# Kernel optimization log

Hardware: AMD Instinct MI355X
Metric: run time of the kernel (lower is better)

## Reference

```python
import jax, jax.numpy as jnp
import numpy as np

H_IMG = 256; W_IMG = 256; C = 256
WIN = (16, 16); STRIPE = (32, 32); DF = 4; NH = 4
ASZ = (STRIPE[0] // DF, STRIPE[1] // DF)
TS = ((STRIPE[0] + ASZ[0]) // 2, (STRIPE[1] + ASZ[1]) // 2)  # stripe bias table half-size (20,20)


def _win_part(x, ws):
    # (B,H,W,c) -> (B*nW, ws0*ws1, c)
    B, H, W, c = x.shape
    x = x.reshape(B, H // ws[0], ws[0], W // ws[1], ws[1], c)
    return x.transpose(0, 1, 3, 2, 4, 5).reshape(-1, ws[0] * ws[1], c)


def _win_rev(w, ws, H, W):
    c = w.shape[-1]
    B = w.shape[0] // ((H // ws[0]) * (W // ws[1]))
    x = w.reshape(B, H // ws[0], W // ws[1], ws[0], ws[1], c)
    return x.transpose(0, 1, 3, 2, 4, 5).reshape(B, H, W, c)


def _l2n(x):
    # F.normalize(dim=-1)
    return x / jnp.maximum(jnp.linalg.norm(x, axis=-1, keepdims=True), 1e-12)


def _affine(attn, logit_scale, w1, b1, w2, table, index):
    # attn: (B_, nH, N1, N2); AffineTransform with mask=None
    N1, N2 = attn.shape[-2], attn.shape[-1]
    attn = attn * jnp.exp(jnp.minimum(logit_scale, np.log(100.0)))  # clamp max=log(1/0.01)
    bt = jax.nn.relu(table.reshape(-1, 2) @ w1 + b1) @ w2  # (T, nH)
    bias = bt[index.reshape(-1)].reshape(N1, N2, -1).transpose(2, 0, 1)  # (nH,N1,N2)
    return attn + (16.0 * jax.nn.sigmoid(bias))[None]


def _coords(start, size):
    h = np.arange(start[0], start[0] + size[0])
    w = np.arange(start[1], start[1] + size[1])
    return np.stack(np.meshgrid(h, w, indexing='ij')).reshape(2, -1)


def _idx(c1, c2, md):
    d = (c1[:, :, None] - c2[:, None, :]).transpose(1, 2, 0).astype(np.int64)
    return (d[..., 0] + md[0] - 1) * (2 * md[1] - 1) + (d[..., 1] + md[1] - 1)


def _table(ts):
    h = np.arange(-(ts[0] - 1), ts[0], dtype=np.float32) / (ts[0] - 1)
    w = np.arange(-(ts[1] - 1), ts[1], dtype=np.float32) / (ts[1] - 1)
    t = np.stack(np.meshgrid(h, w, indexing='ij'), axis=-1)[None] * 8.0
    return (np.sign(t) * np.log2(np.abs(t) + 1.0) / np.log2(8.0)).astype(np.float32)


def setup_inputs():
    ks = iter(jax.random.split(jax.random.key(0), 32))
    def nrm(shape, s=0.02):
        return jax.random.normal(next(ks), shape, dtype=jnp.float32) * s
    inp = {}
    inp['x'] = jax.random.normal(next(ks), (1, H_IMG * W_IMG, C), dtype=jnp.float32)
    inp['qkv_w'] = nrm((C, 3 * C)); inp['qkv_b'] = nrm((3 * C,))
    inp['anchor_w'] = nrm((C, C // 2)); inp['anchor_b'] = nrm((C // 2,))
    for tag in ['w', 's1', 's2']:
        inp['ls_' + tag] = jnp.full((NH, 1, 1), np.log(10.0), dtype=jnp.float32)
        inp['cpb_w1_' + tag] = nrm((2, 512), 0.1)
        inp['cpb_b1_' + tag] = nrm((512,), 0.1)
        inp['cpb_w2_' + tag] = nrm((512, NH), 0.1)
    inp['proj_w'] = nrm((C, C)); inp['proj_b'] = nrm((C,))
    inp['table_w'] = jnp.asarray(_table(WIN))
    inp['table_s'] = jnp.asarray(_table(TS))
    cw = _coords((0, 0), WIN)
    inp['index_w'] = jnp.asarray(_idx(cw, cw, WIN), dtype=jnp.int32)
    cs = _coords((0, 0), STRIPE)
    st = ((STRIPE[0] - ASZ[0]) // 2, (STRIPE[1] - ASZ[1]) // 2)
    ca = _coords(st, ASZ)
    inp['index_a2w'] = jnp.asarray(_idx(ca, cs, TS), dtype=jnp.int32)
    inp['index_w2a'] = jnp.asarray(_idx(cs, ca, TS), dtype=jnp.int32)
    return inp


def reference(x, qkv_w, qkv_b, anchor_w, anchor_b,
              ls_w, cpb_w1_w, cpb_b1_w, cpb_w2_w,
              ls_s1, cpb_w1_s1, cpb_b1_s1, cpb_w2_s1,
              ls_s2, cpb_w1_s2, cpb_b1_s2, cpb_w2_s2,
              proj_w, proj_b, table_w, table_s,
              index_w, index_a2w, index_w2a):
    B, L, c = x.shape
    qkv = x @ qkv_w + qkv_b               # (B, L, 3C)
    half = 3 * c // 2
    hd = half // 3 // NH                  # head_dim per branch
    # ---- window attention on first half of qkv channels ----
    qw = _win_part(qkv[..., :half].reshape(B, H_IMG, W_IMG, half), WIN)  # (B_, N, 3*C/2)
    B_, N, _ = qw.shape
    q, k, v = qw.reshape(B_, N, 3, NH, hd).transpose(2, 0, 3, 1, 4)
    attn = jnp.einsum('bhnd,bhmd->bhnm', _l2n(q), _l2n(k))
    attn = jax.nn.softmax(_affine(attn, ls_w, cpb_w1_w, cpb_b1_w, cpb_w2_w, table_w, index_w), axis=-1)
    xw = jnp.einsum('bhnm,bhmd->bhnd', attn, v).transpose(0, 2, 1, 3).reshape(B_, N, NH * hd)
    xw = _win_rev(xw, WIN, H_IMG, W_IMG).reshape(B, L, c // 2)
    # ---- anchor projection: AvgPool2d(DF) + Linear(C -> C/2) ----
    xi = x.reshape(B, H_IMG, W_IMG, c)
    pooled = xi.reshape(B, H_IMG // DF, DF, W_IMG // DF, DF, c).mean(axis=(2, 4))
    anchor = pooled @ anchor_w + anchor_b  # (B, H/DF, W/DF, C/2)
    # ---- anchor stripe attention on second half ----
    qs = _win_part(qkv[..., half:].reshape(B, H_IMG, W_IMG, half), STRIPE)  # (Bs, N1, 3*C/2)
    Bs, N1, _ = qs.shape
    anc = _win_part(anchor, ASZ)           # (Bs, N2, C/2)
    N2 = anc.shape[1]
    q, k, v = qs.reshape(Bs, N1, 3, NH, hd).transpose(2, 0, 3, 1, 4)
    anc = anc.reshape(Bs, N2, NH, hd).transpose(0, 2, 1, 3)
    a1 = jnp.einsum('bhnd,bhmd->bhnm', _l2n(anc), _l2n(k))   # (Bs,NH,N2,N1)
    a1 = jax.nn.softmax(_affine(a1, ls_s1, cpb_w1_s1, cpb_b1_s1, cpb_w2_s1, table_s, index_a2w), axis=-1)
    xm = jnp.einsum('bhnm,bhmd->bhnd', a1, v)                # (Bs,NH,N2,hd)
    a2 = jnp.einsum('bhnd,bhmd->bhnm', _l2n(q), _l2n(anc))   # (Bs,NH,N1,N2)
    a2 = jax.nn.softmax(_affine(a2, ls_s2, cpb_w1_s2, cpb_b1_s2, cpb_w2_s2, table_s, index_w2a), axis=-1)
    xs = jnp.einsum('bhnm,bhmd->bhnd', a2, xm).transpose(0, 2, 1, 3).reshape(Bs, N1, NH * hd)
    xs = _win_rev(xs, STRIPE, H_IMG, W_IMG).reshape(B, L, c // 2)
    # ---- merge + output projection ----
    return jnp.concatenate([xw, xs], axis=-1) @ proj_w + proj_b
```

## Files before the change

### kernel.cpp

```cpp
#include <hip/hip_runtime.h>
#include <cstdint>
#include <cstddef>

typedef unsigned short u16;
typedef __attribute__((ext_vector_type(8))) short short8;
typedef __attribute__((ext_vector_type(4))) float floatx4;
typedef __attribute__((ext_vector_type(2))) float floatx2;
typedef __attribute__((ext_vector_type(4))) unsigned int uintx4;
typedef __attribute__((ext_vector_type(2))) unsigned int uintx2;
typedef __attribute__((ext_vector_type(2))) __bf16 bf16x2;

#define LOG2E 1.44269504f

__device__ __forceinline__ float bf2f(u16 u){
  union { unsigned int i; float f; } v; v.i = ((unsigned int)u) << 16; return v.f;
}
__device__ __forceinline__ u16 f2bf(float f){
  union { __bf16 b; u16 u; } v; v.b = (__bf16)f; return v.u;
}
__device__ __forceinline__ unsigned int pk2(float a, float b){
  union { bf16x2 h; unsigned int u; } v;
  v.h = __builtin_convertvector((floatx2){a, b}, bf16x2);
  return v.u;
}
__device__ __forceinline__ void gload16(const void* g, void* l){
  __builtin_amdgcn_global_load_lds((const __attribute__((address_space(1))) unsigned int*)g,
                                   (__attribute__((address_space(3))) unsigned int*)l, 16, 0, 0);
}
__device__ __forceinline__ float redq(float v){
  v += __shfl_xor(v, 16); v += __shfl_xor(v, 32);
  return v;
}

__global__ void transpose_w(const float* __restrict__ qkv_w, const float* __restrict__ anchor_w,
                            const float* __restrict__ proj_w,
                            u16* __restrict__ qkvt, u16* __restrict__ anct, u16* __restrict__ projt){
  int id = blockIdx.x*256 + threadIdx.x;
  if (id < 196608){ int k = id / 768, n = id % 768; qkvt[n*256 + k] = f2bf(qkv_w[id]); }
  else if (id < 229376){ int r = id - 196608; int k = r / 128, n = r % 128; anct[n*256 + k] = f2bf(anchor_w[r]); }
  else { int r = id - 229376; int k = r >> 8, n = r & 255; projt[n*256 + k] = f2bf(proj_w[r]); }
}

__global__ void cpb_mlp(const float* __restrict__ tw, const float* __restrict__ ts,
                        const float* __restrict__ w1w, const float* __restrict__ b1w, const float* __restrict__ w2w,
                        const float* __restrict__ w1s1, const float* __restrict__ b1s1, const float* __restrict__ w2s1,
                        const float* __restrict__ w1s2, const float* __restrict__ b1s2, const float* __restrict__ w2s2,
                        float* __restrict__ btw, float* __restrict__ bts1, float* __restrict__ bts2){
  int tag = blockIdx.y;
  const float *tab, *w1, *b1, *w2; float* bt; int T;
  if (tag == 0){ tab = tw; w1 = w1w;  b1 = b1w;  w2 = w2w;  bt = btw;  T = 961; }
  else if (tag == 1){ tab = ts; w1 = w1s1; b1 = b1s1; w2 = w2s1; bt = bts1; T = 1521; }
  else { tab = ts; w1 = w1s2; b1 = b1s2; w2 = w2s2; bt = bts2; T = 1521; }
  __shared__ float sw1[2][512];
  __shared__ float sb1[512];
  __shared__ float sw2[512][4];
  for (int j = threadIdx.x; j < 512; j += 256){
    sw1[0][j] = w1[j]; sw1[1][j] = w1[512 + j]; sb1[j] = b1[j];
    for (int h = 0; h < 4; ++h) sw2[j][h] = w2[j*4 + h];
  }
  __syncthreads();
  int idx = blockIdx.x*256 + threadIdx.x;
  int r = idx >> 2, hh = idx & 3;
  if (r < T){
    float t0 = tab[2*r], t1 = tab[2*r + 1];
    float acc = 0.f;
    for (int j = 0; j < 512; ++j){
      float hj = fmaxf(fmaf(t0, sw1[0][j], fmaf(t1, sw1[1][j], sb1[j])), 0.f);
      acc = fmaf(hj, sw2[j][hh], acc);
    }
    bt[r*4 + hh] = acc;
  }
}

__global__ void bias_gather(const float* __restrict__ btw, const float* __restrict__ bts1,
                            const float* __restrict__ bts2,
                            const int* __restrict__ idxw, const int* __restrict__ idxa2w,
                            const int* __restrict__ idxw2a,
                            const float* __restrict__ lsw, const float* __restrict__ ls1,
                            const float* __restrict__ ls2,
                            float* __restrict__ bw, float* __restrict__ bs1, float* __restrict__ bs2){
  int id = blockIdx.x*256 + threadIdx.x;
  int which = id >> 18;
  int rem = id & 262143;
  int h = rem >> 16, e = rem & 65535;
  const float* bt; const int* ix; float* dst; const float* ls;
  if (which == 0){ bt = btw;  ix = idxw;   dst = bw;  ls = lsw; }
  else if (which == 1){ bt = bts1; ix = idxa2w; dst = bs1; ls = ls1; }
  else { bt = bts2; ix = idxw2a; dst = bs2; ls = ls2; }
  float v = bt[ix[e]*4 + h];
  float scale = exp2f(fminf(ls[h], 4.6051702f) * LOG2E);
  float off = fminf(scale + 16.f, 80.f);
  float sig = 16.f / (1.f + exp2f(-v * LOG2E));
  float out = (sig - off) * LOG2E;
  int idx;
  if (which == 0){
    int q = e >> 8, k = e & 255;
    idx = ((((h*8 + (k>>5))*2 + ((k>>4)&1))*4 + ((k>>2)&3)) << 10) + (q << 2) + (k & 3);
  } else if (which == 1){
    int a = e >> 10, k = e & 1023;
    idx = (((h*64 + (k>>4))*4 + ((k>>2)&3)) << 8) + (a << 2) + (k & 3);
  } else {
    int q = e >> 6, k = e & 63;
    idx = (((h*4 + (k>>4))*4 + ((k>>2)&3)) << 12) + (q << 2) + (k & 3);
  }
  dst[idx] = out;
}

__global__ void avgpool(const float* __restrict__ x, u16* __restrict__ xb,
                        u16* __restrict__ pooledb){
  int a = blockIdx.x, c = threadIdx.x;
  int ay = a >> 6, ax = a & 63;
  float acc = 0.f;
#pragma unroll
  for (int dy = 0; dy < 4; ++dy)
#pragma unroll
    for (int dx = 0; dx < 4; ++dx){
      int row = (ay*4 + dy)*256 + ax*4 + dx;
      float v = x[(size_t)row*256 + c];
      xb[(size_t)row*256 + c] = f2bf(v);
      acc += v;
    }
  pooledb[(size_t)a*256 + c] = f2bf(acc * 0.0625f);
}

__launch_bounds__(256, 2)
__global__ void gemm_bf(const u16* __restrict__ A, const u16* __restrict__ Bt,
                        const float* __restrict__ bias, u16* __restrict__ CW,
                        u16* __restrict__ CS, int Nstr, int nyb, int normSl){
  __shared__ __align__(16) u16 lsA[2][4096];
  __shared__ __align__(16) u16 lsB[2][4096];
  const int tid = threadIdx.x, lane = tid & 63, wv = tid >> 6;
  const int lane15 = lane & 15, quad = lane >> 4;
  const int wr = wv >> 1, wc = wv & 1;
  const int m0 = blockIdx.x * 128;
  const int y = blockIdx.y;
  const int br = y / nyb, sl = y - br*nyb;
  u16* C = br ? CS : CW;
  const int srow = wv*16 + (lane >> 2), sk = (lane & 3)*8;
  const u16* as = A + (size_t)(m0 + srow)*256 + sk;
  const u16* bs = Bt + (size_t)(y*128 + srow)*256 + sk;
  auto stage = [&](int kw, int buf){
    char* dA = (char*)lsA[buf]; char* dB = (char*)lsB[buf];
    gload16(as + kw*32,            dA + wv*1024);
    gload16(as + 64*256 + kw*32,   dA + 4096 + wv*1024);
    gload16(bs + kw*32,            dB + wv*1024);
    gload16(bs + 64*256 + kw*32,   dB + 4096 + wv*1024);
  };
  stage(0, 0);
  floatx4 acc[4][4] = {};
  for (int kw = 0; kw < 8; ++kw){
    __syncthreads();
    if (kw < 7) stage(kw + 1, (kw + 1) & 1);
    const char* Ac = (const char*)lsA[kw & 1];
    const char* Bc = (const char*)lsB[kw & 1];
    short8 a[4], b[4];
#pragma unroll
    for (int i = 0; i < 4; ++i)
      a[i] = *(const short8*)(Ac + (wr*64 + i*16 + lane15)*64 + quad*16);
#pragma unroll
    for (int j = 0; j < 4; ++j)
      b[j] = *(const short8*)(Bc + (wc*64 + j*16 + lane15)*64 + quad*16);
#pragma unroll
    for (int i = 0; i < 4; ++i)
#pragma unroll
      for (int j = 0; j < 4; ++j)
        acc[i][j] = __builtin_amdgcn_mfma_f32_16x16x32_bf16(b[j], a[i], acc[i][j], 0, 0, 0);
  }
#pragma unroll
  for (int j = 0; j < 4; ++j){
    floatx4 bz = *(const floatx4*)(bias + y*128 + wc*64 + j*16 + quad*4);
#pragma unroll
    for (int i = 0; i < 4; ++i) acc[i][j] += bz;
  }
  if (sl < normSl){
#pragma unroll
    for (int i = 0; i < 4; ++i)
#pragma unroll
      for (int jp = 0; jp < 2; ++jp){
        floatx4 s2 = acc[i][jp*2]*acc[i][jp*2] + acc[i][jp*2+1]*acc[i][jp*2+1];
        float ss = (s2.x + s2.y) + (s2.z + s2.w);
        ss = redq(ss);
        float inv = 1.f / fmaxf(sqrtf(ss), 1e-12f);
        acc[i][jp*2]   *= inv;
        acc[i][jp*2+1] *= inv;
      }
  }
#pragma unroll
  for (int i = 0; i < 4; ++i){
    int row = m0 + wr*64 + i*16 + lane15;
#pragma unroll
    for (int j = 0; j < 4; ++j){
      int colb = sl*128 + wc*64 + j*16 + quad*4;
      uintx2 w;
      w.x = pk2(acc[i][j][0], acc[i][j][1]);
      w.y = pk2(acc[i][j][2], acc[i][j][3]);
      *(uintx2*)(C + (size_t)row*Nstr + colb) = w;
    }
  }
}

__launch_bounds__(256, 2)
__global__ void gemm_proj(const u16* __restrict__ Ab, const u16* __restrict__ Bt,
                          const float* __restrict__ bias, float* __restrict__ Cout){
  __shared__ __align__(16) u16 lsA[2][4096];
  __shared__ __align__(16) u16 lsB[2][8192];
  const int tid = threadIdx.x, lane = tid & 63, wv = tid >> 6;
  const int lane15 = lane & 15, quad = lane >> 4;
  const int wr = wv >> 1, wc = wv & 1;
  const int m0 = blockIdx.x * 128;
  const int srow = wv*16 + (lane >> 2), sk = (lane & 3)*8;
  const u16* as = Ab + (size_t)(m0 + srow)*256 + sk;
  const u16* bs = Bt + (size_t)srow*256 + sk;
  auto stage = [&](int kw, int buf){
    char* dA = (char*)lsA[buf]; char* dB = (char*)lsB[buf];
    gload16(as + kw*32,             dA + wv*1024);
    gload16(as + 64*256 + kw*32,    dA + 4096  + wv*1024);
    gload16(bs + kw*32,             dB + wv*1024);
    gload16(bs + 64*256 + kw*32,    dB + 4096  + wv*1024);
    gload16(bs + 128*256 + kw*32,   dB + 8192  + wv*1024);
    gload16(bs + 192*256 + kw*32,   dB + 12288 + wv*1024);
  };
  stage(0, 0);
  floatx4 acc[4][8] = {};
  for (int kw = 0; kw < 8; ++kw){
    __syncthreads();
    if (kw < 7) stage(kw + 1, (kw + 1) & 1);
    const char* Ac = (const char*)lsA[kw & 1];
    const char* Bc = (const char*)lsB[kw & 1];
    short8 a[4], b[8];
#pragma unroll
    for (int i = 0; i < 4; ++i)
      a[i] = *(const short8*)(Ac + (wr*64 + i*16 + lane15)*64 + quad*16);
#pragma unroll
    for (int j = 0; j < 8; ++j)
      b[j] = *(const short8*)(Bc + (wc*128 + j*16 + lane15)*64 + quad*16);
#pragma unroll
    for (int i = 0; i < 4; ++i)
#pragma unroll
      for (int j = 0; j < 8; ++j)
        acc[i][j] = __builtin_amdgcn_mfma_f32_16x16x32_bf16(b[j], a[i], acc[i][j], 0, 0, 0);
  }
#pragma unroll
  for (int i = 0; i < 4; ++i){
    int row = m0 + wr*64 + i*16 + lane15;
#pragma unroll
    for (int j = 0; j < 8; ++j){
      int colb = wc*128 + j*16 + quad*4;
      floatx4 bz = *(const floatx4*)(bias + colb);
      floatx4 o = acc[i][j] + bz;
      *(floatx4*)(Cout + (size_t)row*256 + colb) = o;
    }
  }
}

__launch_bounds__(256, 3)
__global__ void win_attn(const u16* __restrict__ qkvh, const float* __restrict__ lsw,
                         const float* __restrict__ biasw, u16* __restrict__ outm){
  __shared__ __align__(16) u16 sm[24832];
  const int tid = threadIdx.x, lane = tid & 63, wv = tid >> 6;
  const int lane15 = lane & 15, quad = lane >> 4;
  const int h = blockIdx.y;
  const int wyl = blockIdx.x >> 4, wx = blockIdx.x & 15;
  u16* Ks = sm;
  u16* Qs = sm + 8192;
  u16* VT = sm + 16384;
  {
    int tok = wv*64 + lane;
    int row = (wyl*16 + (tok >> 4))*256 + wx*16 + (tok & 15);
    const char* src = (const char*)qkvh + (size_t)row*768 + h*64;
#pragma unroll
    for (int kq = 0; kq < 4; ++kq){
      gload16(src + kq*16,        (char*)Qs + wv*1024 + kq*4096);
      gload16(src + 256 + kq*16,  (char*)Ks + wv*1024 + kq*4096);
    }
    int vrow = (wyl*16 + (tid >> 4))*256 + wx*16 + (tid & 15);
    const uintx4* vp = (const uintx4*)((const char*)qkvh + (size_t)vrow*768 + 512 + h*64);
    uintx4 v0 = vp[0], v1 = vp[1], v2 = vp[2], v3 = vp[3];
    unsigned int w[16] = {v0.x,v0.y,v0.z,v0.w, v1.x,v1.y,v1.z,v1.w,
                          v2.x,v2.y,v2.z,v2.w, v3.x,v3.y,v3.z,v3.w};
    u16* vd = VT + (tid >> 3)*264 + (tid & 7);
#pragma unroll
    for (int c = 0; c < 16; ++c){
      vd[(c*2)*8]   = (u16)(w[c] & 0xffffu);
      vd[(c*2+1)*8] = (u16)(w[c] >> 16);
    }
  }
  __syncthreads();
  short8 qf[4];
#pragma unroll
  for (int j = 0; j < 4; ++j)
    qf[j] = *(const short8*)(Qs + quad*2048 + (wv*64 + j*16 + lane15)*8);
  __syncthreads();

  float scale = exp2f(fminf(lsw[h], 4.6051702f) * LOG2E) * LOG2E;
  u16* Pw = Qs + wv*2048;
  const floatx4 zf4 = {0.f, 0.f, 0.f, 0.f};
  floatx4 accO[2][4] = {};
  float lsum[4] = {};

  for (int kc = 0; kc < 8; ++kc){
    floatx4 bia[2][4];
#pragma unroll
    for (int i = 0; i < 2; ++i)
#pragma unroll
      for (int j = 0; j < 4; ++j)
        bia[i][j] = *(const floatx4*)(biasw + ((((h*8 + kc)*2 + i)*4 + quad) << 10)
                                            + ((wv*64 + j*16 + lane15) << 2));
    short8 kf[2];
#pragma unroll
    for (int i = 0; i < 2; ++i)
      kf[i] = *(const short8*)(Ks + quad*2048 + (kc*32 + i*16 + lane15)*8);
#pragma unroll
    for (int i = 0; i < 2; ++i)
#pragma unroll
      for (int j = 0; j < 4; ++j){
        floatx4 sv = __builtin_amdgcn_mfma_f32_16x16x32_bf16(kf[i], qf[j], zf4, 0, 0, 0);
        float p0 = exp2f(fmaf(sv[0], scale, bia[i][j][0]));
        float p1 = exp2f(fmaf(sv[1], scale, bia[i][j][1]));
        float p2 = exp2f(fmaf(sv[2], scale, bia[i][j][2]));
        float p3 = exp2f(fmaf(sv[3], scale, bia[i][j][3]));
        lsum[j] += (p0 + p1) + (p2 + p3);
        uintx2 w; w.x = pk2(p0, p1); w.y = pk2(p2, p3);
        *(uintx2*)(Pw + (i*2 + (quad>>1))*512 + (j*16 + lane15)*8 + (quad&1)*4) = w;
      }
    asm volatile("s_waitcnt lgkmcnt(0)" ::: "memory");
    short8 ptf[4], vtf[2];
#pragma unroll
    for (int j = 0; j < 4; ++j)
      ptf[j] = *(const short8*)(Pw + quad*512 + (j*16 + lane15)*8);
#pragma unroll
    for (int m = 0; m < 2; ++m)
      vtf[m] = *(const short8*)(VT + (kc*4 + quad)*264 + (m*16 + lane15)*8);
#pragma unroll
    for (int m = 0; m < 2; ++m)
#pragma unroll
      for (int j = 0; j < 4; ++j)
        accO[m][j] = __builtin_amdgcn_mfma_f32_16x16x32_bf16(vtf[m], ptf[j], accO[m][j], 0, 0, 0);
  }
  float linv[4];
#pragma unroll
  for (int j = 0; j < 4; ++j) linv[j] = 1.f / redq(lsum[j]);
#pragma unroll
  for (int m = 0; m < 2; ++m)
#pragma unroll
    for (int j = 0; j < 4; ++j){
      int tok = wv*64 + j*16 + lane15;
      int py = wyl*16 + (tok >> 4), px = wx*16 + (tok & 15);
      floatx4 o = accO[m][j] * linv[j];
      uintx2 w; w.x = pk2(o[0], o[1]); w.y = pk2(o[2], o[3]);
      *(uintx2*)(outm + (size_t)(py*256 + px)*256 + h*32 + m*16 + quad*4) = w;
    }
}

__launch_bounds__(256, 3)
__global__ void stripe_xm(const u16* __restrict__ qkvh, const u16* __restrict__ anchor,
                          const float* __restrict__ ls1, const float* __restrict__ bias1,
                          float* __restrict__ gl1, u16* __restrict__ gO){
  __shared__ __align__(16) u16 sm[22784];
  const int tid = threadIdx.x, lane = tid & 63, wv = tid >> 6;
  const int lane15 = lane & 15, quad = lane >> 4;
  const int s = blockIdx.x, h = blockIdx.y, kb = blockIdx.z;
  const int syl = s >> 3, sx = s & 7;
  u16* ANC = sm; u16* VT = sm + 10240; u16* P1T = sm + 14592;
  if (wv == 0){
    int ay = syl*8 + (lane >> 3), ax = sx*8 + (lane & 7);
    const char* asrc = (const char*)anchor + (size_t)(ay*64 + ax)*256 + h*64;
#pragma unroll
    for (int kq = 0; kq < 4; ++kq)
      gload16(asrc + kq*16, (char*)ANC + kq*1024);
  }
  auto stageK = [&](int kc){
    int kkb = kb*512 + kc*128;
    char* KC = (char*)sm + 4096 + (kc & 1)*8192;
#pragma unroll
    for (int hf = 0; hf < 2; ++hf){
      int tok = kkb + hf*64 + lane;
      int row = (syl*32 + (tok >> 5))*256 + sx*32 + (tok & 31);
      gload16((const char*)qkvh + (size_t)row*768 + 256 + h*64 + wv*16,
              KC + wv*2048 + hf*1024);
    }
  };
  stageK(0);
  float scale1 = exp2f(fminf(ls1[h], 4.6051702f) * LOG2E) * LOG2E;
  const floatx4 zf4 = {0.f, 0.f, 0.f, 0.f};
  floatx4 accO1[2] = {};
  float l1 = 0.f;
  for (int kc = 0; kc < 4; ++kc){
    int kkb = kb*512 + kc*128;
    {
      int tok_l = tid >> 1, dh = tid & 1;
      int tok = kkb + tok_l;
      int row = (syl*32 + (tok >> 5))*256 + sx*32 + (tok & 31);
      const uintx4* vp = (const uintx4*)((const char*)qkvh + (size_t)row*768 + 512 + h*64 + dh*32);
      uintx4 v0 = vp[0], v1 = vp[1];
      unsigned int w[8] = {v0.x,v0.y,v0.z,v0.w, v1.x,v1.y,v1.z,v1.w};
      u16* vd = VT + (tok_l >> 3)*272 + dh*136 + (tok_l & 7);
#pragma unroll
      for (int c = 0; c < 8; ++c){
        vd[(c*2)*8]   = (u16)(w[c] & 0xffffu);
        vd[(c*2+1)*8] = (u16)(w[c] >> 16);
      }
    }
    __syncthreads();
    if (kc < 3) stageK(kc + 1);
    const u16* KC = sm + 2048 + (kc & 1)*4096;
    short8 ancf = *(const short8*)(ANC + quad*512 + (wv*16 + lane15)*8);
    floatx4 bia[8];
#pragma unroll
    for (int i = 0; i < 8; ++i)
      bia[i] = *(const floatx4*)(bias1 + (((h*64 + kb*32 + kc*8 + i)*4 + quad) << 8)
                                       + ((wv*16 + lane15) << 2));
#pragma unroll
    for (int i = 0; i < 8; ++i){
      short8 kf = *(const short8*)(KC + quad*1024 + (i*16 + lane15)*8);
      floatx4 sv = __builtin_amdgcn_mfma_f32_16x16x32_bf16(kf, ancf, zf4, 0, 0, 0);
      float p0 = exp2f(fmaf(sv[0], scale1, bia[i][0]));
      float p1 = exp2f(fmaf(sv[1], scale1, bia[i][1]));
      float p2 = exp2f(fmaf(sv[2], scale1, bia[i][2]));
      float p3 = exp2f(fmaf(sv[3], scale1, bia[i][3]));
      l1 += (p0 + p1) + (p2 + p3);
      uintx2 w; w.x = pk2(p0, p1); w.y = pk2(p2, p3);
      *(uintx2*)(P1T + (i*2 + (quad>>1))*512 + (wv*16 + lane15)*8 + (quad&1)*4) = w;
    }
    asm volatile("s_waitcnt lgkmcnt(0)" ::: "memory");
#pragma unroll
    for (int ks = 0; ks < 4; ++ks){
      short8 ptf = *(const short8*)(P1T + (ks*4 + quad)*512 + (wv*16 + lane15)*8);
#pragma unroll
      for (int m = 0; m < 2; ++m){
        short8 vtf = *(const short8*)(VT + (ks*4 + quad)*272 + m*136 + lane15*8);
        accO1[m] = __builtin_amdgcn_mfma_f32_16x16x32_bf16(vtf, ptf, accO1[m], 0, 0, 0);
      }
    }
    __syncthreads();
  }
  l1 = redq(l1);
  int ent = (s*4 + h)*2 + kb;
  if (quad == 0) gl1[ent*64 + wv*16 + lane15] = l1;
#pragma unroll
  for (int m = 0; m < 2; ++m){
    uintx2 w; w.x = pk2(accO1[m][0], accO1[m][1]); w.y = pk2(accO1[m][2], accO1[m][3]);
    *(uintx2*)(gO + (size_t)ent*2048 + (wv*16 + lane15)*32 + m*16 + quad*4) = w;
  }
}

__launch_bounds__(256, 3)
__global__ void stripe_xs(const u16* __restrict__ qkvh, const u16* __restrict__ anchor,
                          const float* __restrict__ ls2, const float* __restrict__ bias2,
                          const float* __restrict__ gl1, const u16* __restrict__ gO,
                          u16* __restrict__ outm){
  __shared__ __align__(16) u16 sm[20480];
  const int tid = threadIdx.x, lane = tid & 63, wv = tid >> 6;
  const int lane15 = lane & 15, quad = lane >> 4;
  const int s = blockIdx.x >> 2, qc = blockIdx.x & 3, h = blockIdx.y;
  const int syl = s >> 3, sx = s & 7;
  u16* ANC = sm;
  u16* XMT = sm + 2048;
  u16* QW  = sm + 4096 + wv*2048;
  u16* P2T = sm + 12288 + wv*2048;
  if (wv == 0){
    int ay = syl*8 + (lane >> 3), ax = sx*8 + (lane & 7);
    const char* asrc = (const char*)anchor + (size_t)(ay*64 + ax)*256 + h*64;
#pragma unroll
    for (int kq = 0; kq < 4; ++kq)
      gload16(asrc + kq*16, (char*)ANC + kq*1024);
  }
  {
    int a = tid >> 2, db = (tid & 3)*8;
    int e0 = (s*4 + h)*2;
    float inv = 1.f / (gl1[e0*64 + a] + gl1[(e0 + 1)*64 + a]);
    uintx4 u0 = *(const uintx4*)(gO + (size_t)e0*2048 + a*32 + db);
    uintx4 u1 = *(const uintx4*)(gO + (size_t)(e0 + 1)*2048 + a*32 + db);
    unsigned int w0[4] = {u0.x, u0.y, u0.z, u0.w};
    unsigned int w1[4] = {u1.x, u1.y, u1.z, u1.w};
#pragma unroll
    for (int c = 0; c < 4; ++c){
      float a0 = bf2f((u16)(w0[c] & 0xffffu)) + bf2f((u16)(w1[c] & 0xffffu));
      float a1 = bf2f((u16)(w0[c] >> 16))     + bf2f((u16)(w1[c] >> 16));
      XMT[(a >> 3)*256 + (db + c*2)*8     + (a & 7)] = f2bf(a0 * inv);
      XMT[(a >> 3)*256 + (db + c*2 + 1)*8 + (a & 7)] = f2bf(a1 * inv);
    }
  }
  int tq = qc*256 + wv*64;
  {
    int tok = tq + lane;
    int row = (syl*32 + (tok >> 5))*256 + sx*32 + (tok & 31);
    const char* src = (const char*)qkvh + (size_t)row*768 + h*64;
#pragma unroll
    for (int kq = 0; kq < 4; ++kq)
      gload16(src + kq*16, (char*)QW + kq*1024);
  }
  __syncthreads();
  short8 qf2[4];
#pragma unroll
  for (int j = 0; j < 4; ++j)
    qf2[j] = *(const short8*)(QW + quad*512 + (j*16 + lane15)*8);
  float scale2 = exp2f(fminf(ls2[h], 4.6051702f) * LOG2E) * LOG2E;
  const floatx4 zf4 = {0.f, 0.f, 0.f, 0.f};
  floatx4 accO2[2][4] = {};
  float l2[4] = {};
#pragma unroll
  for (int c = 0; c < 2; ++c){
    floatx4 bia[2][4];
#pragma unroll
    for (int i = 0; i < 2; ++i)
#pragma unroll
      for (int j = 0; j < 4; ++j)
        bia[i][j] = *(const floatx4*)(bias2 + ((((h*4 + c*2 + i)*4 + quad) << 12)
                                             + ((tq + j*16 + lane15) << 2)));
    short8 af[2];
#pragma unroll
    for (int i = 0; i < 2; ++i)
      af[i] = *(const short8*)(ANC + quad*512 + (c*32 + i*16 + lane15)*8);
#pragma unroll
    for (int i = 0; i < 2; ++i)
#pragma unroll
      for (int j = 0; j < 4; ++j){
        floatx4 sv = __builtin_amdgcn_mfma_f32_16x16x32_bf16(af[i], qf2[j], zf4, 0, 0, 0);
        float p0 = exp2f(fmaf(sv[0], scale2, bia[i][j][0]));
        float p1 = exp2f(fmaf(sv[1], scale2, bia[i][j][1]));
        float p2 = exp2f(fmaf(sv[2], scale2, bia[i][j][2]));
        float p3 = exp2f(fmaf(sv[3], scale2, bia[i][j][3]));
        l2[j] += (p0 + p1) + (p2 + p3);
        uintx2 w; w.x = pk2(p0, p1); w.y = pk2(p2, p3);
        *(uintx2*)(P2T + (i*2 + (quad>>1))*512 + (j*16 + lane15)*8 + (quad&1)*4) = w;
      }
    asm volatile("s_waitcnt lgkmcnt(0)" ::: "memory");
    short8 ptf[4], xmf[2];
#pragma unroll
    for (int j = 0; j < 4; ++j)
      ptf[j] = *(const short8*)(P2T + quad*512 + (j*16 + lane15)*8);
#pragma unroll
    for (int m = 0; m < 2; ++m)
      xmf[m] = *(const short8*)(XMT + (c*4 + quad)*256 + (m*16 + lane15)*8);
#pragma unroll
    for (int m = 0; m < 2; ++m)
#pragma unroll
      for (int j = 0; j < 4; ++j)
        accO2[m][j] = __builtin_amdgcn_mfma_f32_16x16x32_bf16(xmf[m], ptf[j], accO2[m][j], 0, 0, 0);
  }
  float linv[4];
#pragma unroll
  for (int j = 0; j < 4; ++j) linv[j] = 1.f / redq(l2[j]);
#pragma unroll
  for (int m = 0; m < 2; ++m)
#pragma unroll
    for (int j = 0; j < 4; ++j){
      int tok = tq + j*16 + lane15;
      int py = syl*32 + (tok >> 5), px = sx*32 + (tok & 31);
      floatx4 o = accO2[m][j] * linv[j];
      uintx2 w; w.x = pk2(o[0], o[1]); w.y = pk2(o[2], o[3]);
      *(uintx2*)(outm + (size_t)(py*256 + px)*256 + 128 + h*32 + m*16 + quad*4) = w;
    }
}

extern "C" void kernel_launch(void* const* d_in, const int* in_sizes, int n_in,
                              void* d_out, int out_size, void* d_ws, size_t ws_size,
                              hipStream_t stream) {
  (void)in_sizes; (void)n_in; (void)out_size; (void)ws_size;
  const float* x        = (const float*)d_in[0];
  const float* qkv_w    = (const float*)d_in[1];
  const float* qkv_b    = (const float*)d_in[2];
  const float* anchor_w = (const float*)d_in[3];
  const float* anchor_b = (const float*)d_in[4];
  const float* ls_w     = (const float*)d_in[5];
  const float* w1_w     = (const float*)d_in[6];
  const float* b1_w     = (const float*)d_in[7];
  const float* w2_w     = (const float*)d_in[8];
  const float* ls_s1    = (const float*)d_in[9];
  const float* w1_s1    = (const float*)d_in[10];
  const float* b1_s1    = (const float*)d_in[11];
  const float* w2_s1    = (const float*)d_in[12];
  const float* ls_s2    = (const float*)d_in[13];
  const float* w1_s2    = (const float*)d_in[14];
  const float* b1_s2    = (const float*)d_in[15];
  const float* w2_s2    = (const float*)d_in[16];
  const float* proj_w   = (const float*)d_in[17];
  const float* proj_b   = (const float*)d_in[18];
  const float* table_w  = (const float*)d_in[19];
  const float* table_s  = (const float*)d_in[20];
  const int* index_w   = (const int*)d_in[21];
  const int* index_a2w = (const int*)d_in[22];
  const int* index_w2a = (const int*)d_in[23];

  char* ws = (char*)d_ws;
  u16*   qkvhW  = (u16*)(ws + 0);
  u16*   qkvhS  = (u16*)(ws + 50331648);
  u16*   mergedb= (u16*)(ws + 100663296);
  u16*   xb     = (u16*)(ws + 134217728);
  u16*   pooledb= (u16*)(ws + 167772160);
  u16*   anch   = (u16*)(ws + 169869312);
  u16*   qkvt   = (u16*)(ws + 170917888);
  u16*   anct   = (u16*)(ws + 171311104);
  u16*   projt  = (u16*)(ws + 171376640);
  float* btw    = (float*)(ws + 171507712);
  float* bts1   = (float*)(ws + 171524096);
  float* bts2   = (float*)(ws + 171548672);
  float* biasw  = (float*)(ws + 171573248);
  float* bias1  = (float*)(ws + 172621824);
  float* bias2  = (float*)(ws + 173670400);
  float* gl1    = (float*)(ws + 174718976);
  u16*   gO     = (u16*)(ws + 174850048);

  transpose_w<<<1152, 256, 0, stream>>>(qkv_w, anchor_w, proj_w, qkvt, anct, projt);
  cpb_mlp<<<dim3(24, 3), 256, 0, stream>>>(table_w, table_s,
                                           w1_w, b1_w, w2_w,
                                           w1_s1, b1_s1, w2_s1,
                                           w1_s2, b1_s2, w2_s2,
                                           btw, bts1, bts2);
  bias_gather<<<3072, 256, 0, stream>>>(btw, bts1, bts2, index_w, index_a2w, index_w2a,
                                        ls_w, ls_s1, ls_s2, biasw, bias1, bias2);
  avgpool<<<4096, 256, 0, stream>>>(x, xb, pooledb);
  gemm_bf<<<dim3(32, 1), 256, 0, stream>>>(pooledb, anct, anchor_b, anch, anch, 128, 1, 1);
  gemm_bf<<<dim3(512, 6), 256, 0, stream>>>(xb, qkvt, qkv_b, qkvhW, qkvhS, 384, 3, 2);
  win_attn<<<dim3(256, 4), 256, 0, stream>>>(qkvhW, ls_w, biasw, mergedb);
  stripe_xm<<<dim3(64, 4, 2), 256, 0, stream>>>(qkvhS, anch, ls_s1, bias1, gl1, gO);
  stripe_xs<<<dim3(256, 4), 256, 0, stream>>>(qkvhS, anch, ls_s2, bias2, gl1, gO, mergedb);
  gemm_proj<<<512, 256, 0, stream>>>(mergedb, projt, proj_b, (float*)d_out);
}
```

Baseline: 351.0 us.

## Merge prep kernels and the two projection GEMMs, stage GEMM output through LDS

Weight transpose, CPB MLP and avgpool are merged into a single prep_all launch, and the anchor GEMM and QKV GEMM are merged into one gemm_all grid with an extra y-slice. This removes several kernel launches and their serialization gaps. The GEMM epilogue now writes the tile to LDS and then stores 16-byte coalesced rows. Launch bounds are raised to 4 blocks per CU for the GEMM and 3 for the projection, which puts more pressure on registers. The y=6 slice launches 512 blocks, and all but 32 exit immediately.

New measurement: 349.6 us. About the same (-0.4%).

```diff
diff --git a/kernel.cpp b/kernel.cpp
--- a/kernel.cpp
+++ b/kernel.cpp
@@ -32,43 +32,62 @@
   return v;
 }
 
-__global__ void transpose_w(const float* __restrict__ qkv_w, const float* __restrict__ anchor_w,
-                            const float* __restrict__ proj_w,
-                            u16* __restrict__ qkvt, u16* __restrict__ anct, u16* __restrict__ projt){
-  int id = blockIdx.x*256 + threadIdx.x;
-  if (id < 196608){ int k = id / 768, n = id % 768; qkvt[n*256 + k] = f2bf(qkv_w[id]); }
-  else if (id < 229376){ int r = id - 196608; int k = r / 128, n = r % 128; anct[n*256 + k] = f2bf(anchor_w[r]); }
-  else { int r = id - 229376; int k = r >> 8, n = r & 255; projt[n*256 + k] = f2bf(proj_w[r]); }
-}
-
-__global__ void cpb_mlp(const float* __restrict__ tw, const float* __restrict__ ts,
-                        const float* __restrict__ w1w, const float* __restrict__ b1w, const float* __restrict__ w2w,
-                        const float* __restrict__ w1s1, const float* __restrict__ b1s1, const float* __restrict__ w2s1,
-                        const float* __restrict__ w1s2, const float* __restrict__ b1s2, const float* __restrict__ w2s2,
-                        float* __restrict__ btw, float* __restrict__ bts1, float* __restrict__ bts2){
-  int tag = blockIdx.y;
-  const float *tab, *w1, *b1, *w2; float* bt; int T;
-  if (tag == 0){ tab = tw; w1 = w1w;  b1 = b1w;  w2 = w2w;  bt = btw;  T = 961; }
-  else if (tag == 1){ tab = ts; w1 = w1s1; b1 = b1s1; w2 = w2s1; bt = bts1; T = 1521; }
-  else { tab = ts; w1 = w1s2; b1 = b1s2; w2 = w2s2; bt = bts2; T = 1521; }
+__global__ void prep_all(const float* __restrict__ x,
+                         const float* __restrict__ qkv_w, const float* __restrict__ anchor_w,
+                         const float* __restrict__ proj_w,
+                         const float* __restrict__ tw, const float* __restrict__ ts,
+                         const float* __restrict__ w1w, const float* __restrict__ b1w, const float* __restrict__ w2w,
+                         const float* __restrict__ w1s1, const float* __restrict__ b1s1, const float* __restrict__ w2s1,
+                         const float* __restrict__ w1s2, const float* __restrict__ b1s2, const float* __restrict__ w2s2,
+                         u16* __restrict__ qkvt, u16* __restrict__ anct, u16* __restrict__ projt,
+                         float* __restrict__ btw, float* __restrict__ bts1, float* __restrict__ bts2,
+                         u16* __restrict__ xb, u16* __restrict__ pooledb){
   __shared__ float sw1[2][512];
   __shared__ float sb1[512];
   __shared__ float sw2[512][4];
-  for (int j = threadIdx.x; j < 512; j += 256){
-    sw1[0][j] = w1[j]; sw1[1][j] = w1[512 + j]; sb1[j] = b1[j];
-    for (int h = 0; h < 4; ++h) sw2[j][h] = w2[j*4 + h];
-  }
-  __syncthreads();
-  int idx = blockIdx.x*256 + threadIdx.x;
-  int r = idx >> 2, hh = idx & 3;
-  if (r < T){
-    float t0 = tab[2*r], t1 = tab[2*r + 1];
+  const int bid = blockIdx.x;
+  if (bid < 1152){
+    int id = bid*256 + threadIdx.x;
+    if (id < 196608){ int k = id / 768, n = id % 768; qkvt[n*256 + k] = f2bf(qkv_w[id]); }
+    else if (id < 229376){ int r = id - 196608; int k = r / 128, n = r % 128; anct[n*256 + k] = f2bf(anchor_w[r]); }
+    else { int r = id - 229376; int k = r >> 8, n = r & 255; projt[n*256 + k] = f2bf(proj_w[r]); }
+  } else if (bid < 1224){
+    int cb = bid - 1152;
+    int tag = cb / 24, xb24 = cb % 24;
+    const float *tab, *w1, *b1, *w2; float* bt; int T;
+    if (tag == 0){ tab = tw; w1 = w1w;  b1 = b1w;  w2 = w2w;  bt = btw;  T = 961; }
+    else if (tag == 1){ tab = ts; w1 = w1s1; b1 = b1s1; w2 = w2s1; bt = bts1; T = 1521; }
+    else { tab = ts; w1 = w1s2; b1 = b1s2; w2 = w2s2; bt = bts2; T = 1521; }
+    for (int j = threadIdx.x; j < 512; j += 256){
+      sw1[0][j] = w1[j]; sw1[1][j] = w1[512 + j]; sb1[j] = b1[j];
+      for (int h = 0; h < 4; ++h) sw2[j][h] = w2[j*4 + h];
+    }
+    __syncthreads();
+    int idx = xb24*256 + threadIdx.x;
+    int r = idx >> 2, hh = idx & 3;
+    if (r < T){
+      float t0 = tab[2*r], t1 = tab[2*r + 1];
+      float acc = 0.f;
+      for (int j = 0; j < 512; ++j){
+        float hj = fmaxf(fmaf(t0, sw1[0][j], fmaf(t1, sw1[1][j], sb1[j])), 0.f);
+        acc = fmaf(hj, sw2[j][hh], acc);
+      }
+      bt[r*4 + hh] = acc;
+    }
+  } else {
+    int a = bid - 1224, c = threadIdx.x;
+    int ay = a >> 6, ax = a & 63;
     float acc = 0.f;
-    for (int j = 0; j < 512; ++j){
-      float hj = fmaxf(fmaf(t0, sw1[0][j], fmaf(t1, sw1[1][j], sb1[j])), 0.f);
-      acc = fmaf(hj, sw2[j][hh], acc);
-    }
-    bt[r*4 + hh] = acc;
+#pragma unroll
+    for (int dy = 0; dy < 4; ++dy)
+#pragma unroll
+      for (int dx = 0; dx < 4; ++dx){
+        int row = (ay*4 + dy)*256 + ax*4 + dx;
+        float v = x[(size_t)row*256 + c];
+        xb[(size_t)row*256 + c] = f2bf(v);
+        acc += v;
+      }
+    pooledb[(size_t)a*256 + c] = f2bf(acc * 0.0625f);
   }
 }
 
@@ -106,41 +125,32 @@
   dst[idx] = out;
 }
 
-__global__ void avgpool(const float* __restrict__ x, u16* __restrict__ xb,
-                        u16* __restrict__ pooledb){
-  int a = blockIdx.x, c = threadIdx.x;
-  int ay = a >> 6, ax = a & 63;
-  float acc = 0.f;
-#pragma unroll
-  for (int dy = 0; dy < 4; ++dy)
-#pragma unroll
-    for (int dx = 0; dx < 4; ++dx){
-      int row = (ay*4 + dy)*256 + ax*4 + dx;
-      float v = x[(size_t)row*256 + c];
-      xb[(size_t)row*256 + c] = f2bf(v);
-      acc += v;
-    }
-  pooledb[(size_t)a*256 + c] = f2bf(acc * 0.0625f);
-}
-
-__launch_bounds__(256, 2)
-__global__ void gemm_bf(const u16* __restrict__ A, const u16* __restrict__ Bt,
-                        const float* __restrict__ bias, u16* __restrict__ CW,
-                        u16* __restrict__ CS, int Nstr, int nyb, int normSl){
-  __shared__ __align__(16) u16 lsA[2][4096];
-  __shared__ __align__(16) u16 lsB[2][4096];
+__launch_bounds__(256, 4)
+__global__ void gemm_all(const u16* __restrict__ xb, const u16* __restrict__ pooledb,
+                         const u16* __restrict__ qkvt, const u16* __restrict__ anct,
+                         const float* __restrict__ qkv_b, const float* __restrict__ anchor_b,
+                         u16* __restrict__ CW, u16* __restrict__ CS, u16* __restrict__ anch){
+  __shared__ __align__(16) u16 smem[17408];
   const int tid = threadIdx.x, lane = tid & 63, wv = tid >> 6;
   const int lane15 = lane & 15, quad = lane >> 4;
   const int wr = wv >> 1, wc = wv & 1;
+  const int y = blockIdx.y;
   const int m0 = blockIdx.x * 128;
-  const int y = blockIdx.y;
-  const int br = y / nyb, sl = y - br*nyb;
-  u16* C = br ? CS : CW;
+  const u16 *Ap, *Btp; const float* bp; u16* C; int Nst, sl, nrm;
+  if (y == 6){
+    if (blockIdx.x >= 32) return;
+    Ap = pooledb; Btp = anct; bp = anchor_b; C = anch; Nst = 128; sl = 0; nrm = 1;
+  } else {
+    Ap = xb; Btp = qkvt + (size_t)y*128*256; bp = qkv_b + y*128;
+    C = (y < 3) ? CW : CS; Nst = 384; sl = y % 3; nrm = (sl < 2);
+  }
+  char* base = (char*)smem;
   const int srow = wv*16 + (lane >> 2), sk = (lane & 3)*8;
-  const u16* as = A + (size_t)(m0 + srow)*256 + sk;
-  const u16* bs = Bt + (size_t)(y*128 + srow)*256 + sk;
+  const u16* as = Ap + (size_t)(m0 + srow)*256 + sk;
+  const u16* bs = Btp + (size_t)srow*256 + sk;
   auto stage = [&](int kw, int buf){
-    char* dA = (char*)lsA[buf]; char* dB = (char*)lsB[buf];
+    char* dA = base + buf*8192;
+    char* dB = base + 16384 + buf*8192;
     gload16(as + kw*32,            dA + wv*1024);
     gload16(as + 64*256 + kw*32,   dA + 4096 + wv*1024);
     gload16(bs + kw*32,            dB + wv*1024);
@@ -151,8 +161,8 @@
   for (int kw = 0; kw < 8; ++kw){
     __syncthreads();
     if (kw < 7) stage(kw + 1, (kw + 1) & 1);
-    const char* Ac = (const char*)lsA[kw & 1];
-    const char* Bc = (const char*)lsB[kw & 1];
+    const char* Ac = base + (kw & 1)*8192;
+    const char* Bc = base + 16384 + (kw & 1)*8192;
     short8 a[4], b[4];
 #pragma unroll
     for (int i = 0; i < 4; ++i)
@@ -168,11 +178,11 @@
   }
 #pragma unroll
   for (int j = 0; j < 4; ++j){
-    floatx4 bz = *(const floatx4*)(bias + y*128 + wc*64 + j*16 + quad*4);
+    floatx4 bz = *(const floatx4*)(bp + wc*64 + j*16 + quad*4);
 #pragma unroll
     for (int i = 0; i < 4; ++i) acc[i][j] += bz;
   }
-  if (sl < normSl){
+  if (nrm){
 #pragma unroll
     for (int i = 0; i < 4; ++i)
 #pragma unroll
@@ -185,21 +195,30 @@
         acc[i][jp*2+1] *= inv;
       }
   }
+  __syncthreads();
 #pragma unroll
   for (int i = 0; i < 4; ++i){
-    int row = m0 + wr*64 + i*16 + lane15;
+    int rl = wr*64 + i*16 + lane15;
 #pragma unroll
     for (int j = 0; j < 4; ++j){
-      int colb = sl*128 + wc*64 + j*16 + quad*4;
+      int col = wc*64 + j*16 + quad*4;
       uintx2 w;
       w.x = pk2(acc[i][j][0], acc[i][j][1]);
       w.y = pk2(acc[i][j][2], acc[i][j][3]);
-      *(uintx2*)(C + (size_t)row*Nstr + colb) = w;
-    }
-  }
-}
-
-__launch_bounds__(256, 2)
+      *(uintx2*)(smem + rl*136 + col) = w;
+    }
+  }
+  __syncthreads();
+  const int r0 = tid >> 4, seg = tid & 15;
+#pragma unroll
+  for (int it = 0; it < 8; ++it){
+    int r = it*16 + r0;
+    uintx4 w = *(const uintx4*)(smem + r*136 + seg*8);
+    *(uintx4*)(C + (size_t)(m0 + r)*Nst + sl*128 + seg*8) = w;
+  }
+}
+
+__launch_bounds__(256, 3)
 __global__ void gemm_proj(const u16* __restrict__ Ab, const u16* __restrict__ Bt,
                           const float* __restrict__ bias, float* __restrict__ Cout){
   __shared__ __align__(16) u16 lsA[2][4096];
@@ -602,17 +621,14 @@
   float* gl1    = (float*)(ws + 174718976);
   u16*   gO     = (u16*)(ws + 174850048);
 
-  transpose_w<<<1152, 256, 0, stream>>>(qkv_w, anchor_w, proj_w, qkvt, anct, projt);
-  cpb_mlp<<<dim3(24, 3), 256, 0, stream>>>(table_w, table_s,
-                                           w1_w, b1_w, w2_w,
-                                           w1_s1, b1_s1, w2_s1,
-                                           w1_s2, b1_s2, w2_s2,
-                                           btw, bts1, bts2);
+  prep_all<<<5320, 256, 0, stream>>>(x, qkv_w, anchor_w, proj_w, table_w, table_s,
+                                     w1_w, b1_w, w2_w, w1_s1, b1_s1, w2_s1,
+                                     w1_s2, b1_s2, w2_s2,
+                                     qkvt, anct, projt, btw, bts1, bts2, xb, pooledb);
   bias_gather<<<3072, 256, 0, stream>>>(btw, bts1, bts2, index_w, index_a2w, index_w2a,
                                         ls_w, ls_s1, ls_s2, biasw, bias1, bias2);
-  avgpool<<<4096, 256, 0, stream>>>(x, xb, pooledb);
-  gemm_bf<<<dim3(32, 1), 256, 0, stream>>>(pooledb, anct, anchor_b, anch, anch, 128, 1, 1);
-  gemm_bf<<<dim3(512, 6), 256, 0, stream>>>(xb, qkvt, qkv_b, qkvhW, qkvhS, 384, 3, 2);
+  gemm_all<<<dim3(512, 7), 256, 0, stream>>>(xb, pooledb, qkvt, anct, qkv_b, anchor_b,
+                                             qkvhW, qkvhS, anch);
   win_attn<<<dim3(256, 4), 256, 0, stream>>>(qkvhW, ls_w, biasw, mergedb);
   stripe_xm<<<dim3(64, 4, 2), 256, 0, stream>>>(qkvhS, anch, ls_s1, bias1, gl1, gO);
   stripe_xs<<<dim3(256, 4), 256, 0, stream>>>(qkvhS, anch, ls_s2, bias2, gl1, gO, mergedb);
```
